# Kernel tuning notes

Hardware: AMD Instinct MI355X
Metric: run time of the kernel (lower is better)

## Reference

```python
import jax, jax.numpy as jnp
import numpy as np

N_NODES = 10000
N_EDGES = 160000
G = 64  # num graphs in batch
D_IN, D_HID, D_OUT = 1280, 512, 256
EPS = 1e-12


def setup_inputs() -> dict:
    key = jax.random.key(0)
    ks = jax.random.split(key, 16)
    x = jax.random.normal(ks[0], (N_NODES, D_IN), dtype=jnp.float32)
    edge_index = jax.random.randint(ks[1], (2, N_EDGES), 0, N_NODES, dtype=jnp.int64)
    batch = jnp.sort(jax.random.randint(ks[2], (N_NODES,), 0, G, dtype=jnp.int64))
    vector = jax.random.normal(ks[3], (G, D_OUT), dtype=jnp.float32)
    s = 0.02
    p = {
        'W1': jax.random.normal(ks[4], (D_IN, D_HID), dtype=jnp.float32) * s,
        'b1': jnp.zeros((D_HID,), jnp.float32),
        'W2': jax.random.normal(ks[5], (D_HID, D_HID), dtype=jnp.float32) * s,
        'b2': jnp.zeros((D_HID,), jnp.float32),
        'W3': jax.random.normal(ks[6], (D_HID, D_HID), dtype=jnp.float32) * s,
        'b3': jnp.zeros((D_HID,), jnp.float32),
        'W4': jax.random.normal(ks[7], (D_HID, D_OUT), dtype=jnp.float32) * s,
        'b4': jnp.zeros((D_OUT,), jnp.float32),
        'cW1': jax.random.normal(ks[8], (512, 256), dtype=jnp.float32) * s,
        'cb1': jnp.zeros((256,), jnp.float32),
        'cW2': jax.random.normal(ks[9], (256, 64), dtype=jnp.float32) * s,
        'cb2': jnp.zeros((64,), jnp.float32),
        'cW3': jax.random.normal(ks[10], (64, 1), dtype=jnp.float32) * s,
        'cb3': jnp.zeros((1,), jnp.float32),
    }
    return dict(x=x, edge_index=edge_index, batch=batch, vector=vector, **p)


def _gcn_conv(h, W, b, src, dst, norm):
    # PyG GCNConv: X W, then symmetric-normalized scatter-add over edges (self-loops included)
    h = h @ W
    msg = h[src] * norm[:, None]              # [E+N, d]
    out = jax.ops.segment_sum(msg, dst, num_segments=N_NODES)
    return out + b


def reference(x, edge_index, batch, vector,
              W1, b1, W2, b2, W3, b3, W4, b4,
              cW1, cb1, cW2, cb2, cW3, cb3):
    loops = jnp.arange(N_NODES, dtype=edge_index.dtype)
    src = jnp.concatenate([edge_index[0], loops])
    dst = jnp.concatenate([edge_index[1], loops])
    deg = jax.ops.segment_sum(jnp.ones_like(dst, dtype=x.dtype), dst, num_segments=N_NODES)
    dis = deg ** -0.5                          # deg >= 1 due to self loops
    norm = dis[src] * dis[dst]

    h = _gcn_conv(x, W1, b1, src, dst, norm)
    h = jax.nn.relu(h)                          # dropout is identity in eval
    h = _gcn_conv(h, W2, b2, src, dst, norm)
    h = jax.nn.relu(h)
    h = _gcn_conv(h, W3, b3, src, dst, norm)
    h = jax.nn.relu(h)
    h = _gcn_conv(h, W4, b4, src, dst, norm)

    # global_mean_pool
    sums = jax.ops.segment_sum(h, batch, num_segments=G)
    cnts = jax.ops.segment_sum(jnp.ones((N_NODES,), h.dtype), batch, num_segments=G)
    pool = sums / jnp.maximum(cnts, 1.0)[:, None]
    # F.normalize(dim=1)
    pool = pool / jnp.maximum(jnp.linalg.norm(pool, axis=1, keepdims=True), EPS)

    combined = jnp.concatenate([pool, vector], axis=1)   # [G, 512]
    z = jax.nn.relu(combined @ cW1 + cb1)
    z = jax.nn.relu(z @ cW2 + cb2)
    return jax.nn.sigmoid(z @ cW3 + cb3)                  # [G, 1]
```

## Files before the change

### kernel.cpp

```cpp
#include <hip/hip_runtime.h>
#include <hip/hip_bf16.h>
#include <type_traits>


#define N_NODES 10000
#define N_EDGES 160000
#define NGRAPH  64
#define MPAD    10112
#define PCHUNK  16

typedef __attribute__((ext_vector_type(8))) short short8;
typedef __attribute__((ext_vector_type(4))) float f32x4;
typedef __attribute__((ext_vector_type(4))) unsigned short u16x4;
typedef __attribute__((ext_vector_type(8))) unsigned short u16x8;

__device__ __forceinline__ unsigned short f2bf(float f) {
    unsigned u = __float_as_uint(f);
    return (unsigned short)((u + 0x7FFFu + ((u >> 16) & 1u)) >> 16);
}
__device__ __forceinline__ float bf2f(unsigned short u) {
    return __uint_as_float(((unsigned)u) << 16);
}
__device__ __forceinline__ void gl_lds16(const void* g, void* l) {
    __builtin_amdgcn_global_load_lds(
        (const __attribute__((address_space(1))) unsigned*)g,
        (__attribute__((address_space(3))) unsigned*)l, 16, 0, 0);
}

__global__ __launch_bounds__(256) void zero_i32(int* p, int n) {
    int i = blockIdx.x * 256 + threadIdx.x;
    if (i < n) p[i] = 0;
}
__global__ __launch_bounds__(256) void zero_f32(float* p, int n) {
    int i = blockIdx.x * 256 + threadIdx.x;
    if (i < n) p[i] = 0.0f;
}

__global__ __launch_bounds__(256) void conv_bf16(const float4* __restrict__ in,
                                                 u16x4* __restrict__ out, int n4) {
    int i = blockIdx.x * 256 + threadIdx.x;
    if (i >= n4) return;
    float4 v = in[i];
    u16x4 o;
    o.x = f2bf(v.x); o.y = f2bf(v.y); o.z = f2bf(v.z); o.w = f2bf(v.w);
    out[i] = o;
}

__global__ __launch_bounds__(256) void conv_transpose_w4(
        const float* __restrict__ W1, const float* __restrict__ W2,
        const float* __restrict__ W3, const float* __restrict__ W4,
        unsigned short* __restrict__ W1t, unsigned short* __restrict__ W2t,
        unsigned short* __restrict__ W3t, unsigned short* __restrict__ W4t) {
    const float* W; unsigned short* Wt; int K, N;
    switch (blockIdx.z) {
        case 0:  W = W1; Wt = W1t; K = 1280; N = 512; break;
        case 1:  W = W2; Wt = W2t; K = 512;  N = 512; break;
        case 2:  W = W3; Wt = W3t; K = 512;  N = 512; break;
        default: W = W4; Wt = W4t; K = 512;  N = 256; break;
    }
    int k0 = blockIdx.x * 32, n0 = blockIdx.y * 32;
    if (k0 >= K || n0 >= N) return;
    __shared__ float t[32][33];
    int tx = threadIdx.x & 31, ty = threadIdx.x >> 5;
#pragma unroll
    for (int i = 0; i < 4; i++)
        t[ty + i * 8][tx] = W[(size_t)(k0 + ty + i * 8) * N + n0 + tx];
    __syncthreads();
#pragma unroll
    for (int i = 0; i < 4; i++)
        Wt[(size_t)(n0 + ty + i * 8) * K + k0 + tx] = f2bf(t[tx][ty + i * 8]);
}

__global__ __launch_bounds__(256) void transpose_f32_2(
        const float* __restrict__ cW1, const float* __restrict__ cW2,
        float* __restrict__ cW1t, float* __restrict__ cW2t) {
    const float* W; float* Wt; int K, N;
    if (blockIdx.z == 0) { W = cW1; Wt = cW1t; K = 512; N = 256; }
    else                 { W = cW2; Wt = cW2t; K = 256; N = 64; }
    int k0 = blockIdx.x * 32, n0 = blockIdx.y * 32;
    if (k0 >= K || n0 >= N) return;
    __shared__ float t[32][33];
    int tx = threadIdx.x & 31, ty = threadIdx.x >> 5;
#pragma unroll
    for (int i = 0; i < 4; i++)
        t[ty + i * 8][tx] = W[(size_t)(k0 + ty + i * 8) * N + n0 + tx];
    __syncthreads();
#pragma unroll
    for (int i = 0; i < 4; i++)
        Wt[(size_t)(n0 + ty + i * 8) * K + k0 + tx] = t[tx][ty + i * 8];
}

__global__ __launch_bounds__(256) void deg_count(const int* __restrict__ dst, int* __restrict__ degc, int E) {
    int e = blockIdx.x * 256 + threadIdx.x;
    if (e < E) atomicAdd(&degc[dst[e]], 1);
}

__global__ __launch_bounds__(1024) void scan_offsets(const int* __restrict__ cnt,
                                                     int* __restrict__ off,
                                                     float* __restrict__ dis, int n) {
    __shared__ int wsum[16];
    __shared__ int carry;
    int t = threadIdx.x;
    int wv = t >> 6, ln = t & 63;
    if (t == 0) { carry = 0; off[0] = 0; }
    __syncthreads();
    for (int base = 0; base < n; base += 1024) {
        int idx = base + t;
        int v = (idx < n) ? cnt[idx] : 0;
        if (idx < n) dis[idx] = rsqrtf((float)(v + 1));
#pragma unroll
        for (int o = 1; o < 64; o <<= 1) {
            int u = __shfl_up(v, o);
            if (ln >= o) v += u;
        }
        if (ln == 63) wsum[wv] = v;
        __syncthreads();
        if (wv == 0 && ln < 16) {
            int s = wsum[ln];
#pragma unroll
            for (int o = 1; o < 16; o <<= 1) {
                int u = __shfl_up(s, o);
                if (ln >= o) s += u;
            }
            wsum[ln] = s;
        }
        __syncthreads();
        int add = (wv > 0) ? wsum[wv - 1] : 0;
        int total = wsum[15];
        if (idx < n) off[idx + 1] = v + add + carry;
        __syncthreads();
        if (t == 0) carry += total;
        __syncthreads();
    }
}

__global__ __launch_bounds__(256) void csr_fill(const int* __restrict__ srcI,
                                                const int* __restrict__ dstI,
                                                const int* __restrict__ off,
                                                int* __restrict__ fc,
                                                const float* __restrict__ dis,
                                                int* __restrict__ csr_src,
                                                float* __restrict__ csr_w, int E) {
    int e = blockIdx.x * 256 + threadIdx.x;
    if (e >= E) return;
    int d = dstI[e];
    int s = srcI[e];
    int pos = off[d] + atomicAdd(&fc[d], 1);
    csr_src[pos] = s;
    csr_w[pos] = dis[s];
}

__global__ __launch_bounds__(256) void gemm_bf16(const unsigned short* __restrict__ A,
                                                 const unsigned short* __restrict__ Bt,
                                                 unsigned short* __restrict__ C,
                                                 int K, int N) {
    __shared__ short lA[64 * 64];
    __shared__ short lB[128 * 64];
    int tid = threadIdx.x;
    int lane = tid & 63;
    int wave = tid >> 6;
    int rm = blockIdx.y, cn = blockIdx.x;
    int wr = wave >> 1, wc = wave & 1;

    f32x4 acc[2][4];
#pragma unroll
    for (int m = 0; m < 2; m++)
#pragma unroll
        for (int n = 0; n < 4; n++) acc[m][n] = (f32x4){0.f, 0.f, 0.f, 0.f};

    int lrow = lane >> 3;
    int lcs = ((lane & 7) ^ (lrow & 7)) * 8;

    for (int k0 = 0; k0 < K; k0 += 64) {
        __syncthreads();
#pragma unroll
        for (int i = 0; i < 2; i++) {
            int s = wave * 2 + i;
            int row = rm * 64 + s * 8 + lrow;
            if (row > N_NODES - 1) row = N_NODES - 1;
            gl_lds16(A + (size_t)row * K + k0 + lcs, &lA[s * 512]);
        }
#pragma unroll
        for (int i = 0; i < 4; i++) {
            int s = wave * 4 + i;
            int row = cn * 128 + s * 8 + lrow;
            gl_lds16(Bt + (size_t)row * K + k0 + lcs, &lB[s * 512]);
        }
        __syncthreads();
#pragma unroll
        for (int kk = 0; kk < 64; kk += 32) {
            int cbase = (kk >> 3) + (lane >> 4);
            short8 a[2], b[4];
#pragma unroll
            for (int m = 0; m < 2; m++) {
                int r = wr * 32 + m * 16 + (lane & 15);
                a[m] = *(const short8*)&lA[r * 64 + (cbase ^ (r & 7)) * 8];
            }
#pragma unroll
            for (int n = 0; n < 4; n++) {
                int r = wc * 64 + n * 16 + (lane & 15);
                b[n] = *(const short8*)&lB[r * 64 + (cbase ^ (r & 7)) * 8];
            }
#pragma unroll
            for (int m = 0; m < 2; m++)
#pragma unroll
                for (int n = 0; n < 4; n++)
                    acc[m][n] = __builtin_amdgcn_mfma_f32_16x16x32_bf16(a[m], b[n], acc[m][n], 0, 0, 0);
        }
    }
    int r0 = rm * 64 + wr * 32 + (lane >> 4) * 4;
    int c0 = cn * 128 + wc * 64 + (lane & 15);
#pragma unroll
    for (int m = 0; m < 2; m++)
#pragma unroll
        for (int n = 0; n < 4; n++)
#pragma unroll
            for (int j = 0; j < 4; j++)
                C[(size_t)(r0 + m * 16 + j) * N + c0 + n * 16] = f2bf(acc[m][n][j]);
}

template<int D, bool RELU, bool OUTBF>
__global__ __launch_bounds__(256) void gather_nodes(const unsigned short* __restrict__ h,
                                                    const int* __restrict__ off,
                                                    const int* __restrict__ csr_src,
                                                    const float* __restrict__ csr_w,
                                                    const float* __restrict__ dis,
                                                    const float* __restrict__ bias,
                                                    void* __restrict__ outp) {
    constexpr int VPL = D / 64;
    using uvec = typename std::conditional<VPL == 8, u16x8, u16x4>::type;
    int n = blockIdx.x * 4 + (threadIdx.x >> 6);
    if (n >= N_NODES) return;
    int lane = threadIdx.x & 63;
    const unsigned short* hl = h + (size_t)lane * VPL;
    float dn = dis[n];
    float acc[VPL];
    uvec sv = *(const uvec*)(hl + (size_t)n * D);
#pragma unroll
    for (int j = 0; j < VPL; j++) acc[j] = dn * bf2f(sv[j]);
    int kb = off[n], ke = off[n + 1];
    int k = kb;
    for (; k + 4 <= ke; k += 4) {
        int s0 = csr_src[k + 0], s1 = csr_src[k + 1], s2 = csr_src[k + 2], s3 = csr_src[k + 3];
        float w0 = csr_w[k + 0], w1 = csr_w[k + 1], w2 = csr_w[k + 2], w3 = csr_w[k + 3];
        uvec v0 = *(const uvec*)(hl + (size_t)s0 * D);
        uvec v1 = *(const uvec*)(hl + (size_t)s1 * D);
        uvec v2 = *(const uvec*)(hl + (size_t)s2 * D);
        uvec v3 = *(const uvec*)(hl + (size_t)s3 * D);
#pragma unroll
        for (int j = 0; j < VPL; j++)
            acc[j] += w0 * bf2f(v0[j]) + w1 * bf2f(v1[j]) + w2 * bf2f(v2[j]) + w3 * bf2f(v3[j]);
    }
    for (; k < ke; k++) {
        int s = csr_src[k];
        float w = csr_w[k];
        uvec v = *(const uvec*)(hl + (size_t)s * D);
#pragma unroll
        for (int j = 0; j < VPL; j++) acc[j] += w * bf2f(v[j]);
    }
#pragma unroll
    for (int j = 0; j < VPL; j++) {
        float o = acc[j] * dn + bias[lane * VPL + j];
        if (RELU) o = fmaxf(o, 0.0f);
        acc[j] = o;
    }
    if (OUTBF) {
        uvec ov;
#pragma unroll
        for (int j = 0; j < VPL; j++) ov[j] = f2bf(acc[j]);
        *(uvec*)((unsigned short*)outp + (size_t)n * D + lane * VPL) = ov;
    } else {
#pragma unroll
        for (int j = 0; j < VPL; j += 4)
            *(float4*)((float*)outp + (size_t)n * D + lane * VPL + j) =
                make_float4(acc[j], acc[j + 1], acc[j + 2], acc[j + 3]);
    }
}

__global__ __launch_bounds__(256) void pool_partial(const float* __restrict__ agg,
                                                    const int* __restrict__ batch,
                                                    float* __restrict__ pool) {
    int c0 = blockIdx.x * PCHUNK;
    int t = threadIdx.x;
    int end = c0 + PCHUNK;
    if (end > N_NODES) end = N_NODES;
    float acc = 0.0f;
    int cur = batch[c0];
    for (int n = c0; n < end; n++) {
        int g = batch[n];
        if (g != cur) {
            atomicAdd(&pool[cur * 256 + t], acc);
            acc = 0.0f;
            cur = g;
        }
        acc += agg[(size_t)n * 256 + t];
    }
    atomicAdd(&pool[cur * 256 + t], acc);
}

__device__ __forceinline__ int lbound(const int* __restrict__ a, int n, int key) {
    int lo = 0, hi = n;
    while (lo < hi) {
        int mid = (lo + hi) >> 1;
        if (a[mid] < key) lo = mid + 1; else hi = mid;
    }
    return lo;
}

__global__ __launch_bounds__(256) void head_comb(const float* __restrict__ pool,
                                                 const int* __restrict__ batch,
                                                 const float* __restrict__ vec,
                                                 float* __restrict__ comb) {
    int g = blockIdx.x;
    int t = threadIdx.x;
    __shared__ float red[4];
    int lo = lbound(batch, N_NODES, g);
    int hi = lbound(batch, N_NODES, g + 1);
    float c = fmaxf((float)(hi - lo), 1.0f);
    float pm = pool[g * 256 + t] / c;

    float ss = pm * pm;
#pragma unroll
    for (int o = 32; o; o >>= 1) ss += __shfl_down(ss, o);
    if ((t & 63) == 0) red[t >> 6] = ss;
    __syncthreads();
    if (t == 0) {
        float tot = red[0] + red[1] + red[2] + red[3];
        red[0] = 1.0f / fmaxf(sqrtf(tot), 1e-12f);
    }
    __syncthreads();
    comb[g * 512 + t] = pm * red[0];
    comb[g * 512 + 256 + t] = vec[g * 256 + t];
}

__global__ __launch_bounds__(256) void head_z1(const float* __restrict__ comb,
                                               const float* __restrict__ cW1t,
                                               const float* __restrict__ cb1,
                                               float* __restrict__ z1) {
    int wid = (blockIdx.x * 256 + threadIdx.x) >> 6;
    int lane = threadIdx.x & 63;
    int g = wid >> 8;
    int o = wid & 255;
    const float4* ca = (const float4*)(comb + g * 512);
    const float4* wa = (const float4*)(cW1t + (size_t)o * 512);
    float s = 0.0f;
#pragma unroll
    for (int r = 0; r < 2; r++) {
        float4 c4 = ca[lane * 2 + r];
        float4 w4 = wa[lane * 2 + r];
        s += c4.x * w4.x + c4.y * w4.y + c4.z * w4.z + c4.w * w4.w;
    }
#pragma unroll
    for (int off = 32; off; off >>= 1) s += __shfl_down(s, off);
    if (lane == 0) z1[g * 256 + o] = fmaxf(s + cb1[o], 0.0f);
}

__global__ __launch_bounds__(256) void head_z2z3(const float* __restrict__ z1,
                                                 const float* __restrict__ cW2t,
                                                 const float* __restrict__ cb2,
                                                 const float* __restrict__ cW3,
                                                 const float* __restrict__ cb3,
                                                 float* __restrict__ out) {
    int g = blockIdx.x;
    int t = threadIdx.x;
    int j = t >> 2;
    int q = t & 3;
    __shared__ float part[256];
    __shared__ float z2s[64];
    const float* z = z1 + g * 256;
    const float* w = cW2t + (size_t)j * 256;
    float s = 0.0f;
#pragma unroll
    for (int i = q * 64; i < q * 64 + 64; i += 4) {
        float4 zv = *(const float4*)(z + i);
        float4 wv = *(const float4*)(w + i);
        s += zv.x * wv.x + zv.y * wv.y + zv.z * wv.z + zv.w * wv.w;
    }
    part[t] = s;
    __syncthreads();
    if (q == 0) {
        float v = part[j * 4] + part[j * 4 + 1] + part[j * 4 + 2] + part[j * 4 + 3] + cb2[j];
        z2s[j] = fmaxf(v, 0.0f);
    }
    __syncthreads();
    if (t < 64) {
        float p = z2s[t] * cW3[t];
#pragma unroll
        for (int off = 32; off; off >>= 1) p += __shfl_down(p, off);
        if (t == 0) out[g] = 1.0f / (1.0f + expf(-(p + cb3[0])));
    }
}

extern "C" void kernel_launch(void* const* d_in, const int* in_sizes, int n_in,
                              void* d_out, int out_size, void* d_ws, size_t ws_size,
                              hipStream_t stream) {
    const float* x   = (const float*)d_in[0];
    const int*   ei  = (const int*)d_in[1];
    const int*   bat = (const int*)d_in[2];
    const float* vec = (const float*)d_in[3];
    const float* W1 = (const float*)d_in[4];
    const float* b1 = (const float*)d_in[5];
    const float* W2 = (const float*)d_in[6];
    const float* b2 = (const float*)d_in[7];
    const float* W3 = (const float*)d_in[8];
    const float* b3 = (const float*)d_in[9];
    const float* W4 = (const float*)d_in[10];
    const float* b4 = (const float*)d_in[11];
    const float* cW1 = (const float*)d_in[12];
    const float* cb1 = (const float*)d_in[13];
    const float* cW2 = (const float*)d_in[14];
    const float* cb2 = (const float*)d_in[15];
    const float* cW3 = (const float*)d_in[16];
    const float* cb3 = (const float*)d_in[17];

    const int* srcI = ei;
    const int* dstI = ei + N_EDGES;

    char* base = (char*)d_ws;
    int*   degc     = (int*)base;              base += N_NODES * 4;
    int*   fc       = (int*)base;              base += N_NODES * 4;
    int*   off      = (int*)base;              base += (N_NODES + 1) * 4 + 4;
    float* dis      = (float*)base;            base += N_NODES * 4;
    int*   csr_src  = (int*)base;              base += N_EDGES * 4;
    float* csr_w    = (float*)base;            base += N_EDGES * 4;
    float* pool     = (float*)base;            base += NGRAPH * 256 * 4;
    float* comb     = (float*)base;            base += NGRAPH * 512 * 4;
    float* z1       = (float*)base;            base += NGRAPH * 256 * 4;
    float* cW1t     = (float*)base;            base += 512 * 256 * 4;
    float* cW2t     = (float*)base;            base += 256 * 64 * 4;
    unsigned short* xb   = (unsigned short*)base;  base += (size_t)N_NODES * 1280 * 2;
    unsigned short* W1t  = (unsigned short*)base;  base += 512 * 1280 * 2;
    unsigned short* W2t  = (unsigned short*)base;  base += 512 * 512 * 2;
    unsigned short* W3t  = (unsigned short*)base;  base += 512 * 512 * 2;
    unsigned short* W4t  = (unsigned short*)base;  base += 256 * 512 * 2;
    unsigned short* h    = (unsigned short*)base;  base += (size_t)MPAD * 512 * 2;
    unsigned short* aggb = (unsigned short*)base;  base += (size_t)N_NODES * 512 * 2;
    float* agg4 = (float*)xb;

    conv_bf16<<<(N_NODES * 1280 / 4 + 255) / 256, 256, 0, stream>>>((const float4*)x, (u16x4*)xb, N_NODES * 1280 / 4);
    conv_transpose_w4<<<dim3(40, 16, 4), 256, 0, stream>>>(W1, W2, W3, W4, W1t, W2t, W3t, W4t);
    transpose_f32_2<<<dim3(16, 8, 2), 256, 0, stream>>>(cW1, cW2, cW1t, cW2t);

    zero_i32<<<(2 * N_NODES + 255) / 256, 256, 0, stream>>>(degc, 2 * N_NODES);
    deg_count<<<(N_EDGES + 255) / 256, 256, 0, stream>>>(dstI, degc, N_EDGES);
    scan_offsets<<<1, 1024, 0, stream>>>(degc, off, dis, N_NODES);
    csr_fill<<<(N_EDGES + 255) / 256, 256, 0, stream>>>(srcI, dstI, off, fc, dis, csr_src, csr_w, N_EDGES);

    gemm_bf16<<<dim3(512 / 128, MPAD / 64), 256, 0, stream>>>(xb, W1t, h, 1280, 512);
    gather_nodes<512, true, true><<<2500, 256, 0, stream>>>(h, off, csr_src, csr_w, dis, b1, aggb);
    gemm_bf16<<<dim3(512 / 128, MPAD / 64), 256, 0, stream>>>(aggb, W2t, h, 512, 512);
    gather_nodes<512, true, true><<<2500, 256, 0, stream>>>(h, off, csr_src, csr_w, dis, b2, aggb);
    gemm_bf16<<<dim3(512 / 128, MPAD / 64), 256, 0, stream>>>(aggb, W3t, h, 512, 512);
    gather_nodes<512, true, true><<<2500, 256, 0, stream>>>(h, off, csr_src, csr_w, dis, b3, aggb);
    gemm_bf16<<<dim3(256 / 128, MPAD / 64), 256, 0, stream>>>(aggb, W4t, h, 512, 256);
    gather_nodes<256, false, false><<<2500, 256, 0, stream>>>(h, off, csr_src, csr_w, dis, b4, agg4);

    zero_f32<<<(NGRAPH * 256 + 255) / 256, 256, 0, stream>>>(pool, NGRAPH * 256);
    pool_partial<<<(N_NODES + PCHUNK - 1) / PCHUNK, 256, 0, stream>>>(agg4, bat, pool);
    head_comb<<<NGRAPH, 256, 0, stream>>>(pool, bat, vec, comb);
    head_z1<<<4096, 256, 0, stream>>>(comb, cW1t, cb1, z1);
    head_z2z3<<<NGRAPH, 256, 0, stream>>>(z1, cW2t, cb2, cW3, cb3, (float*)d_out);
}
```

Baseline: 356.6 us.

## Double-buffer LDS tiles in bf16 GEMM to overlap loads with MFMA

The GEMM kernel now holds two LDS buffers for the A and B tiles. It issues the direct-to-LDS loads for the next K-tile before running the MFMAs on the current one, with a single barrier per iteration. The aim is to hide global-load latency behind matrix compute instead of serialising load, barrier and compute. This doubles LDS use per block, which can lower occupancy, and the barrier at the end of each iteration still waits for the outstanding loads.

```diff
diff --git a/kernel.cpp b/kernel.cpp
--- a/kernel.cpp
+++ b/kernel.cpp
@@ -154,8 +154,8 @@
                                                  const unsigned short* __restrict__ Bt,
                                                  unsigned short* __restrict__ C,
                                                  int K, int N) {
-    __shared__ short lA[64 * 64];
-    __shared__ short lB[128 * 64];
+    __shared__ short lA[2][64 * 64];
+    __shared__ short lB[2][128 * 64];
     int tid = threadIdx.x;
     int lane = tid & 63;
     int wave = tid >> 6;
@@ -171,22 +171,30 @@
     int lrow = lane >> 3;
     int lcs = ((lane & 7) ^ (lrow & 7)) * 8;
 
-    for (int k0 = 0; k0 < K; k0 += 64) {
-        __syncthreads();
-#pragma unroll
-        for (int i = 0; i < 2; i++) {
-            int s = wave * 2 + i;
-            int row = rm * 64 + s * 8 + lrow;
-            if (row > N_NODES - 1) row = N_NODES - 1;
-            gl_lds16(A + (size_t)row * K + k0 + lcs, &lA[s * 512]);
-        }
-#pragma unroll
-        for (int i = 0; i < 4; i++) {
-            int s = wave * 4 + i;
-            int row = cn * 128 + s * 8 + lrow;
-            gl_lds16(Bt + (size_t)row * K + k0 + lcs, &lB[s * 512]);
-        }
-        __syncthreads();
+    int arow = rm * 64 + (wave * 2) * 8 + lrow;
+    int brow = cn * 128 + (wave * 4) * 8 + lrow;
+
+#define STAGE(b, k0)                                                            \
+    {                                                                           \
+        _Pragma("unroll")                                                       \
+        for (int i = 0; i < 2; i++) {                                           \
+            int row = arow + i * 8;                                             \
+            if (row > N_NODES - 1) row = N_NODES - 1;                           \
+            gl_lds16(A + (size_t)row * K + (k0) + lcs, &lA[b][(wave * 2 + i) * 512]); \
+        }                                                                       \
+        _Pragma("unroll")                                                       \
+        for (int i = 0; i < 4; i++) {                                           \
+            int row = brow + i * 8;                                             \
+            gl_lds16(Bt + (size_t)row * K + (k0) + lcs, &lB[b][(wave * 4 + i) * 512]); \
+        }                                                                       \
+    }
+
+    int nt = K >> 6;
+    STAGE(0, 0);
+    __syncthreads();
+    for (int t = 0; t < nt; t++) {
+        int cur = t & 1;
+        if (t + 1 < nt) STAGE((t + 1) & 1, (t + 1) << 6);
 #pragma unroll
         for (int kk = 0; kk < 64; kk += 32) {
             int cbase = (kk >> 3) + (lane >> 4);
@@ -194,12 +202,12 @@
 #pragma unroll
             for (int m = 0; m < 2; m++) {
                 int r = wr * 32 + m * 16 + (lane & 15);
-                a[m] = *(const short8*)&lA[r * 64 + (cbase ^ (r & 7)) * 8];
+                a[m] = *(const short8*)&lA[cur][r * 64 + (cbase ^ (r & 7)) * 8];
             }
 #pragma unroll
             for (int n = 0; n < 4; n++) {
                 int r = wc * 64 + n * 16 + (lane & 15);
-                b[n] = *(const short8*)&lB[r * 64 + (cbase ^ (r & 7)) * 8];
+                b[n] = *(const short8*)&lB[cur][r * 64 + (cbase ^ (r & 7)) * 8];
             }
 #pragma unroll
             for (int m = 0; m < 2; m++)
@@ -207,7 +215,10 @@
                 for (int n = 0; n < 4; n++)
                     acc[m][n] = __builtin_amdgcn_mfma_f32_16x16x32_bf16(a[m], b[n], acc[m][n], 0, 0, 0);
         }
-    }
+        __syncthreads();
+    }
+#undef STAGE
+
     int r0 = rm * 64 + wr * 32 + (lane >> 4) * 4;
     int c0 = cn * 128 + wc * 64 + (lane & 15);
 #pragma unroll
```

After: 359.0 us. No clear change (+0.7%).
